# Kernel optimization log

Measured on AMD Instinct MI355X. Metric: run time of the kernel, lower is better.

The kernel has to match this reference:

```python
import jax, jax.numpy as jnp
import numpy as np

# e2m1 FP4 value table: sign bit in nibble MSB, values {0,0.5,1,1.5,2,3,4,6}
_E2M1 = jnp.array([0.0, 0.5, 1.0, 1.5, 2.0, 3.0, 4.0, 6.0,
                   -0.0, -0.5, -1.0, -1.5, -2.0, -3.0, -4.0, -6.0], dtype=jnp.float32)


def _dequant_fp4(packed, scales, group_size):
    """packed: [E, out, in//8] uint32; scales: [E, in//group_size, out] -> [E, out, in] f32."""
    shifts = jnp.arange(8, dtype=jnp.uint32) * 4  # nibble shift amounts 0,4,...,28
    nib = (packed[..., None] >> shifts) & jnp.uint32(0xF)  # [E, out, in//8, 8]
    E, O, P, _ = nib.shape
    nib = nib.reshape(E, O, P * 8).astype(jnp.int32)
    w = _E2M1[nib]  # [E, out, in] f32
    gids = jnp.arange(P * 8) // group_size  # group id per input column
    sc = jnp.transpose(scales, (0, 2, 1))[:, :, gids]  # [E, out, in]
    return w * sc


def setup_inputs() -> dict:
    E, H, I, T, K, G = 8, 2048, 1408, 2048, 2, 128
    key = jax.random.key(0)
    ks = jax.random.split(key, 9)
    x = jax.random.normal(ks[0], (T, H), dtype=jnp.float32)
    gate_packed = jax.random.bits(ks[1], (E, I, H // 8), dtype=jnp.uint32)
    up_packed = jax.random.bits(ks[2], (E, I, H // 8), dtype=jnp.uint32)
    down_packed = jax.random.bits(ks[3], (E, H, I // 8), dtype=jnp.uint32)
    gate_scales = jax.random.uniform(ks[4], (E, H // G, I), jnp.float32, 0.5, 1.5)
    up_scales = jax.random.uniform(ks[5], (E, H // G, I), jnp.float32, 0.5, 1.5)
    down_scales = jax.random.uniform(ks[6], (E, I // G, H), jnp.float32, 0.5, 1.5)
    topk_idx = jax.random.randint(ks[7], (T, K), 0, E, dtype=jnp.int32)
    w = jax.random.uniform(ks[8], (T, K), jnp.float32)
    topk_w = w / jnp.sum(w, axis=-1, keepdims=True)
    return {"x": x,
            "gate_packed": gate_packed, "gate_scales": gate_scales,
            "up_packed": up_packed, "up_scales": up_scales,
            "down_packed": down_packed, "down_scales": down_scales,
            "topk_idx": topk_idx, "topk_w": topk_w, "group_size": G}


def reference(x, gate_packed, gate_scales, up_packed, up_scales,
              down_packed, down_scales, topk_idx, topk_w, group_size):
    # Fused dequant (nibble unpack + e2m1 table + per-group scale) for all experts
    gate_w = _dequant_fp4(gate_packed, gate_scales, group_size)  # [E, I, H]
    up_w = _dequant_fp4(up_packed, up_scales, group_size)        # [E, I, H]
    down_w = _dequant_fp4(down_packed, down_scales, group_size)  # [E, H, I]
    # Grouped SwiGLU expert MLP (dense over E=8 experts, gather routed outputs)
    g = jnp.einsum('th,eih->eti', x, gate_w)
    u = jnp.einsum('th,eih->eti', x, up_w)
    h = jax.nn.silu(g) * u                                        # [E, T, I]
    y = jnp.einsum('eti,ehi->eth', h, down_w)                     # [E, T, H]
    T = x.shape[0]
    sel = y[topk_idx, jnp.arange(T)[:, None], :]                  # [T, K, H]
    return jnp.sum(sel * topk_w[..., None], axis=1)               # [T, H]
```

## Files before the change

### kernel.cpp

```cpp
#include <hip/hip_runtime.h>
#include <hip/hip_bf16.h>
#include <stdint.h>

#define E_ 8
#define H_ 2048
#define I_ 1408
#define T_ 2048
#define K_ 2
#define G_ 128

typedef __bf16 bf16;
typedef bf16 bf16x8 __attribute__((ext_vector_type(8)));
typedef float f32x4 __attribute__((ext_vector_type(4)));

__device__ __forceinline__ uint32_t prm(uint32_t hi, uint32_t lo, uint32_t sel) {
    return __builtin_amdgcn_perm(hi, lo, sel);
}

struct DequantTab { uint32_t thi0, thi1, tlo0, tlo1; };

__device__ __forceinline__ DequantTab build_tab(float s) {
    union { bf16 h[8]; uint32_t u[4]; } tb;
    tb.h[0] = (bf16)(0.0f);
    tb.h[1] = (bf16)(0.5f * s);
    tb.h[2] = (bf16)(1.0f * s);
    tb.h[3] = (bf16)(1.5f * s);
    tb.h[4] = (bf16)(2.0f * s);
    tb.h[5] = (bf16)(3.0f * s);
    tb.h[6] = (bf16)(4.0f * s);
    tb.h[7] = (bf16)(6.0f * s);
    DequantTab t;
    t.thi0 = prm(tb.u[1], tb.u[0], 0x07050301u);
    t.tlo0 = prm(tb.u[1], tb.u[0], 0x06040200u);
    t.thi1 = prm(tb.u[3], tb.u[2], 0x07050301u);
    t.tlo1 = prm(tb.u[3], tb.u[2], 0x06040200u);
    return t;
}

__device__ __forceinline__ uint4 dequant8t(uint32_t p, const DequantTab& t) {
    const uint32_t pr = p >> 4;
    const uint32_t pe = p  & 0x07070707u;
    const uint32_t po = pr & 0x07070707u;
    const uint32_t He = prm(t.thi1, t.thi0, pe) | ((p  & 0x08080808u) << 4);
    const uint32_t Le = prm(t.tlo1, t.tlo0, pe);
    const uint32_t Ho = prm(t.thi1, t.thi0, po) | ((pr & 0x08080808u) << 4);
    const uint32_t Lo = prm(t.tlo1, t.tlo0, po);
    const uint32_t E01 = prm(He, Le, 0x05010400u);
    const uint32_t E23 = prm(He, Le, 0x07030602u);
    const uint32_t O01 = prm(Ho, Lo, 0x05010400u);
    const uint32_t O23 = prm(Ho, Lo, 0x07030602u);
    return make_uint4(prm(O01, E01, 0x05040100u),
                      prm(O01, E01, 0x07060302u),
                      prm(O23, E23, 0x05040100u),
                      prm(O23, E23, 0x07060302u));
}

__device__ __forceinline__ void gld16(void* lds, const void* g) {
    __builtin_amdgcn_global_load_lds(
        (__attribute__((address_space(1))) void*)g,
        (__attribute__((address_space(3))) void*)lds, 16, 0, 0);
}

__global__ void route_count(const int* __restrict__ topk_idx, int* __restrict__ counts) {
    int p = blockIdx.x * blockDim.x + threadIdx.x;
    if (p < T_ * K_) atomicAdd(&counts[topk_idx[p]], 1);
}

__global__ void route_scan(const int* __restrict__ counts, int* __restrict__ offsets,
                           int* __restrict__ tmap) {
    if (threadIdx.x == 0) {
        int acc = 0, ti = 0;
        for (int e = 0; e < E_; e++) {
            offsets[e] = acc;
            int nt = (counts[e] + 127) >> 7;
            for (int j = 0; j < nt; j++) tmap[ti++] = (e << 16) | j;
            acc += counts[e];
        }
        offsets[E_] = acc;
        for (; ti < 64; ti++) tmap[ti] = -1;
    }
}

__global__ void route_fill(const int* __restrict__ topk_idx, const float* __restrict__ topk_w,
                           int* __restrict__ cursors, const int* __restrict__ offsets,
                           int* __restrict__ tok, float* __restrict__ wgt,
                           int* __restrict__ inv) {
    int p = blockIdx.x * blockDim.x + threadIdx.x;
    if (p < T_ * K_) {
        int e = topk_idx[p];
        int slot = atomicAdd(&cursors[e], 1);
        int idx = offsets[e] + slot;
        tok[idx] = p / K_;
        wgt[idx] = topk_w[p];
        inv[p] = idx;
    }
}

__global__ __launch_bounds__(256)
void xcast_kernel(const float* __restrict__ x, uint4* __restrict__ xb) {
    const int i = blockIdx.x * 256 + threadIdx.x;
    const float4 a = ((const float4*)x)[i * 2];
    const float4 b = ((const float4*)x)[i * 2 + 1];
    union { uint4 u; bf16 h[8]; } r;
    r.h[0] = (bf16)a.x; r.h[1] = (bf16)a.y; r.h[2] = (bf16)a.z; r.h[3] = (bf16)a.w;
    r.h[4] = (bf16)b.x; r.h[5] = (bf16)b.y; r.h[6] = (bf16)b.z; r.h[7] = (bf16)b.w;
    xb[i] = r.u;
}

__global__ __launch_bounds__(256)
void gemm1p_kernel(const bf16* __restrict__ xb,
                   const uint32_t* __restrict__ gate_packed,
                   const float* __restrict__ gate_scales,
                   const uint32_t* __restrict__ up_packed,
                   const float* __restrict__ up_scales,
                   const int* __restrict__ offsets,
                   const int* __restrict__ tmap,
                   const int* __restrict__ tok, bf16* __restrict__ h_buf)
{
    const int tm = tmap[blockIdx.y];
    if (tm < 0) return;
    const int e = tm >> 16, ty = tm & 0xffff;
    const int row0 = offsets[e];
    const int cnt = offsets[e + 1] - row0;
    const int itile = blockIdx.x;

    __shared__ __align__(16) bf16 xs[2][128][32];
    __shared__ __align__(16) bf16 wgs[2][64][32];
    __shared__ __align__(16) bf16 wus[2][64][32];
    __shared__ int toks[128];

    const int tid = threadIdx.x;
    if (tid < 128) {
        int r = ty * 128 + tid;
        toks[tid] = tok[row0 + ((r < cnt) ? r : (cnt - 1))];
    }
    __syncthreads();

    const int srow = tid >> 2;
    const int scol = (tid & 3) * 8;
    const int wcol = tid & 3;
    const size_t t0 = toks[srow], t1 = toks[64 + srow];
    const bf16* xg0 = xb + t0 * H_ + scol;
    const bf16* xg1 = xb + t1 * H_ + scol;
    bf16* lx0[2] = { &xs[0][srow][scol], &xs[1][srow][scol] };
    bf16* lx1[2] = { &xs[0][64 + srow][scol], &xs[1][64 + srow][scol] };

    const int irow = itile * 64 + srow;
    const uint32_t* gp_row = gate_packed + (size_t)e * I_ * (H_ / 8) + (size_t)irow * (H_ / 8) + wcol;
    const uint32_t* up_row = up_packed + (size_t)e * I_ * (H_ / 8) + (size_t)irow * (H_ / 8) + wcol;
    const float* gs_row = gate_scales + (size_t)e * (H_ / G_) * I_ + irow;
    const float* us_row = up_scales + (size_t)e * (H_ / G_) * I_ + irow;
    uint4* lwg[2] = { (uint4*)&wgs[0][srow][wcol * 8], (uint4*)&wgs[1][srow][wcol * 8] };
    uint4* lwu[2] = { (uint4*)&wus[0][srow][wcol * 8], (uint4*)&wus[1][srow][wcol * 8] };

    const int wave = tid >> 6, lane = tid & 63;
    const int wy = wave >> 1, wx = wave & 1;
    const int lrow = lane & 15, kq = lane >> 4;

    f32x4 accg[4][2] = {};
    f32x4 accu[4][2] = {};

    float sg_c = gs_row[0], su_c = us_row[0];
    uint32_t pg0 = gp_row[0], pu0 = up_row[0];
    gld16(lx0[0], xg0);
    gld16(lx1[0], xg1);
    DequantTab tg = build_tab(sg_c), tu = build_tab(su_c);
    *lwg[0] = dequant8t(pg0, tg);
    *lwu[0] = dequant8t(pu0, tu);
    __syncthreads();

    for (int kg = 0; kg < H_ / G_; kg++) {
        float sg_n = 0.f, su_n = 0.f;
        if (kg < H_ / G_ - 1) { sg_n = gs_row[(kg + 1) * I_]; su_n = us_row[(kg + 1) * I_]; }
#pragma unroll
        for (int kk = 0; kk < 4; kk++) {
            const int k = kg * 4 + kk;
            const int b = k & 1, nb = b ^ 1;
            const bool hasn = (k < H_ / 32 - 1);
            uint32_t pgn = 0, pun = 0;
            if (hasn) {
                pgn = gp_row[(k + 1) * 4];
                pun = up_row[(k + 1) * 4];
                gld16(lx0[nb], xg0 + (k + 1) * 32);
                gld16(lx1[nb], xg1 + (k + 1) * 32);
            }
            bf16x8 a[4], bg[2], bu[2];
#pragma unroll
            for (int mi = 0; mi < 4; mi++)
                a[mi] = *(const bf16x8*)&xs[b][wy * 64 + mi * 16 + lrow][kq * 8];
#pragma unroll
            for (int ni = 0; ni < 2; ni++) {
                bg[ni] = *(const bf16x8*)&wgs[b][wx * 32 + ni * 16 + lrow][kq * 8];
                bu[ni] = *(const bf16x8*)&wus[b][wx * 32 + ni * 16 + lrow][kq * 8];
            }
#pragma unroll
            for (int mi = 0; mi < 4; mi++)
#pragma unroll
                for (int ni = 0; ni < 2; ni++) {
                    accg[mi][ni] = __builtin_amdgcn_mfma_f32_16x16x32_bf16(a[mi], bg[ni], accg[mi][ni], 0, 0, 0);
                    accu[mi][ni] = __builtin_amdgcn_mfma_f32_16x16x32_bf16(a[mi], bu[ni], accu[mi][ni], 0, 0, 0);
                }
            if (hasn) {
                if (kk == 3) { tg = build_tab(sg_n); tu = build_tab(su_n); }
                *lwg[nb] = dequant8t(pgn, tg);
                *lwu[nb] = dequant8t(pun, tu);
            }
            __syncthreads();
        }
    }

#pragma unroll
    for (int mi = 0; mi < 4; mi++)
#pragma unroll
        for (int ni = 0; ni < 2; ni++) {
            const int icol = itile * 64 + wx * 32 + ni * 16 + lrow;
#pragma unroll
            for (int r = 0; r < 4; r++) {
                const int grow = ty * 128 + wy * 64 + mi * 16 + kq * 4 + r;
                if (grow < cnt) {
                    const float gv = accg[mi][ni][r];
                    const float hv = gv / (1.f + __expf(-gv)) * accu[mi][ni][r];
                    h_buf[(size_t)(row0 + grow) * I_ + icol] = (bf16)hv;
                }
            }
        }
}

__global__ __launch_bounds__(256)
void gemm2p_kernel(const bf16* __restrict__ h_buf,
                   const uint32_t* __restrict__ down_packed,
                   const float* __restrict__ down_scales,
                   const int* __restrict__ offsets,
                   const int* __restrict__ tmap,
                   const int* __restrict__ tok,
                   const float* __restrict__ wgt, float* __restrict__ yp)
{
    const int tm = tmap[blockIdx.y];
    if (tm < 0) return;
    const int e = tm >> 16, ty = tm & 0xffff;
    const int row0 = offsets[e];
    const int cnt = offsets[e + 1] - row0;
    const int htile = blockIdx.x;

    __shared__ __align__(16) bf16 hs[2][128][32];
    __shared__ __align__(16) bf16 wds[2][128][32];
    __shared__ float wgts[128];

    const int tid = threadIdx.x;
    if (tid < 128) {
        int r = ty * 128 + tid;
        wgts[tid] = (r < cnt) ? wgt[row0 + r] : 0.f;
    }
    __syncthreads();

    const int srow = tid >> 2;
    const int scol = (tid & 3) * 8;
    const int m0 = ty * 128 + srow;
    const int hr0 = row0 + ((m0 < cnt) ? m0 : (cnt - 1));
    const int m1 = m0 + 64;
    const int hr1 = row0 + ((m1 < cnt) ? m1 : (cnt - 1));
    const bf16* hg0 = h_buf + (size_t)hr0 * I_ + scol;
    const bf16* hg1 = h_buf + (size_t)hr1 * I_ + scol;
    bf16* lh0[2] = { &hs[0][srow][scol], &hs[1][srow][scol] };
    bf16* lh1[2] = { &hs[0][64 + srow][scol], &hs[1][64 + srow][scol] };

    const int srow2 = tid >> 1;
    const int wcol2 = (tid & 1) * 2;
    const int hrow = htile * 128 + srow2;
    const uint32_t* dp_row = down_packed + (size_t)e * H_ * (I_ / 8) + (size_t)hrow * (I_ / 8) + wcol2;
    const float* ds_row = down_scales + (size_t)e * (I_ / G_) * H_ + hrow;
    uint4* lwd0[2] = { (uint4*)&wds[0][srow2][wcol2 * 8], (uint4*)&wds[1][srow2][wcol2 * 8] };
    uint4* lwd1[2] = { (uint4*)&wds[0][srow2][wcol2 * 8 + 8], (uint4*)&wds[1][srow2][wcol2 * 8 + 8] };

    const int wave = tid >> 6, lane = tid & 63;
    const int wy = wave >> 1, wx = wave & 1;
    const int lrow = lane & 15, kq = lane >> 4;

    f32x4 acc[4][4] = {};

    float sd_c = ds_row[0];
    uint32_t pd0 = dp_row[0], pd1 = dp_row[1];
    gld16(lh0[0], hg0);
    gld16(lh1[0], hg1);
    DequantTab td = build_tab(sd_c);
    *lwd0[0] = dequant8t(pd0, td);
    *lwd1[0] = dequant8t(pd1, td);
    __syncthreads();

    for (int kg = 0; kg < I_ / G_; kg++) {
        float sd_n = 0.f;
        if (kg < I_ / G_ - 1) sd_n = ds_row[(kg + 1) * H_];
#pragma unroll
        for (int kk = 0; kk < 4; kk++) {
            const int k = kg * 4 + kk;
            const int b = k & 1, nb = b ^ 1;
            const bool hasn = (k < I_ / 32 - 1);
            uint32_t pdn0 = 0, pdn1 = 0;
            if (hasn) {
                pdn0 = dp_row[(k + 1) * 4];
                pdn1 = dp_row[(k + 1) * 4 + 1];
                gld16(lh0[nb], hg0 + (k + 1) * 32);
                gld16(lh1[nb], hg1 + (k + 1) * 32);
            }
            bf16x8 a[4], bb[4];
#pragma unroll
            for (int mi = 0; mi < 4; mi++)
                a[mi] = *(const bf16x8*)&hs[b][wy * 64 + mi * 16 + lrow][kq * 8];
#pragma unroll
            for (int ni = 0; ni < 4; ni++)
                bb[ni] = *(const bf16x8*)&wds[b][wx * 64 + ni * 16 + lrow][kq * 8];
#pragma unroll
            for (int mi = 0; mi < 4; mi++)
#pragma unroll
                for (int ni = 0; ni < 4; ni++)
                    acc[mi][ni] = __builtin_amdgcn_mfma_f32_16x16x32_bf16(a[mi], bb[ni], acc[mi][ni], 0, 0, 0);
            if (hasn) {
                if (kk == 3) td = build_tab(sd_n);
                *lwd0[nb] = dequant8t(pdn0, td);
                *lwd1[nb] = dequant8t(pdn1, td);
            }
            __syncthreads();
        }
    }

#pragma unroll
    for (int mi = 0; mi < 4; mi++)
#pragma unroll
        for (int ni = 0; ni < 4; ni++) {
            const int col = htile * 128 + wx * 64 + ni * 16 + lrow;
#pragma unroll
            for (int r = 0; r < 4; r++) {
                const int lr = wy * 64 + mi * 16 + kq * 4 + r;
                if (ty * 128 + lr < cnt)
                    yp[(size_t)(row0 + ty * 128 + lr) * H_ + col] = acc[mi][ni][r] * wgts[lr];
            }
        }
}

__global__ __launch_bounds__(256)
void combine_kernel(const float* __restrict__ yp, const int* __restrict__ inv,
                    float* __restrict__ out) {
    const int idx = blockIdx.x * 256 + threadIdx.x;
    const int t = idx >> 9;
    const int c = idx & 511;
    const float4 a = ((const float4*)yp)[(size_t)inv[t * 2] * (H_ / 4) + c];
    const float4 b = ((const float4*)yp)[(size_t)inv[t * 2 + 1] * (H_ / 4) + c];
    float4 o;
    o.x = a.x + b.x; o.y = a.y + b.y; o.z = a.z + b.z; o.w = a.w + b.w;
    ((float4*)out)[idx] = o;
}

extern "C" void kernel_launch(void* const* d_in, const int* in_sizes, int n_in,
                              void* d_out, int out_size, void* d_ws, size_t ws_size,
                              hipStream_t stream) {
    const float* x = (const float*)d_in[0];
    const uint32_t* gate_packed = (const uint32_t*)d_in[1];
    const float* gate_scales = (const float*)d_in[2];
    const uint32_t* up_packed = (const uint32_t*)d_in[3];
    const float* up_scales = (const float*)d_in[4];
    const uint32_t* down_packed = (const uint32_t*)d_in[5];
    const float* down_scales = (const float*)d_in[6];
    const int* topk_idx = (const int*)d_in[7];
    const float* topk_w = (const float*)d_in[8];
    float* out = (float*)d_out;

    char* ws = (char*)d_ws;
    int* counts  = (int*)ws;
    int* cursors = (int*)(ws + 32);
    int* offsets = (int*)(ws + 64);
    int* tmap    = (int*)(ws + 128);
    int* tok     = (int*)(ws + 512);
    float* wgt   = (float*)(ws + 16896);
    int* inv     = (int*)(ws + 33280);
    bf16* h_buf  = (bf16*)(ws + 49664);
    bf16* xb     = (bf16*)(ws + 49664 + 11534336ull);
    float* yp    = (float*)(ws + 49664 + 11534336ull + 8388608ull);

    hipMemsetAsync(d_ws, 0, 512, stream);

    route_count<<<(T_ * K_ + 255) / 256, 256, 0, stream>>>(topk_idx, counts);
    route_scan<<<1, 64, 0, stream>>>(counts, offsets, tmap);
    route_fill<<<(T_ * K_ + 255) / 256, 256, 0, stream>>>(topk_idx, topk_w, cursors, offsets,
                                                          tok, wgt, inv);
    xcast_kernel<<<T_ * H_ / 8 / 256, 256, 0, stream>>>(x, (uint4*)xb);

    dim3 g1(I_ / 64, 40);
    gemm1p_kernel<<<g1, 256, 0, stream>>>(xb, gate_packed, gate_scales, up_packed, up_scales,
                                          offsets, tmap, tok, h_buf);
    dim3 g2(H_ / 128, 40);
    gemm2p_kernel<<<g2, 256, 0, stream>>>(h_buf, down_packed, down_scales,
                                          offsets, tmap, tok, wgt, yp);
    combine_kernel<<<T_ * H_ / 4 / 256, 256, 0, stream>>>(yp, inv, out);
}
```

Measured before the change: 333.3 us.

## Replace LDS-staged GEMMs with register-direct loads and smaller row tiles

Both expert GEMMs stop staging activations and dequantized weights through shared memory and drop the per-step barriers. Each wave now loads its A fragments straight from global memory into registers and dequantizes its own B fragments in registers, prefetching one k-step ahead. Row tiles shrink from 128 to 64 tokens (more tiles in tmap, grid y raised to 72), and gemm1 widens its I tile to 128. The trade is that weights and activations are no longer shared across waves through LDS, so global and L2 traffic goes up, and the A loads are uncoalesced gathers by token row.

Result: slower. 494.0 us (+48.2%).

```diff
diff --git a/kernel.cpp b/kernel.cpp
--- a/kernel.cpp
+++ b/kernel.cpp
@@ -37,7 +37,7 @@
     return t;
 }
 
-__device__ __forceinline__ uint4 dequant8t(uint32_t p, const DequantTab& t) {
+__device__ __forceinline__ bf16x8 dequant8t(uint32_t p, const DequantTab& t) {
     const uint32_t pr = p >> 4;
     const uint32_t pe = p  & 0x07070707u;
     const uint32_t po = pr & 0x07070707u;
@@ -49,16 +49,12 @@
     const uint32_t E23 = prm(He, Le, 0x07030602u);
     const uint32_t O01 = prm(Ho, Lo, 0x05010400u);
     const uint32_t O23 = prm(Ho, Lo, 0x07030602u);
-    return make_uint4(prm(O01, E01, 0x05040100u),
-                      prm(O01, E01, 0x07060302u),
-                      prm(O23, E23, 0x05040100u),
-                      prm(O23, E23, 0x07060302u));
-}
-
-__device__ __forceinline__ void gld16(void* lds, const void* g) {
-    __builtin_amdgcn_global_load_lds(
-        (__attribute__((address_space(1))) void*)g,
-        (__attribute__((address_space(3))) void*)lds, 16, 0, 0);
+    union { uint4 u; bf16x8 v; } r;
+    r.u = make_uint4(prm(O01, E01, 0x05040100u),
+                     prm(O01, E01, 0x07060302u),
+                     prm(O23, E23, 0x05040100u),
+                     prm(O23, E23, 0x07060302u));
+    return r.v;
 }
 
 __global__ void route_count(const int* __restrict__ topk_idx, int* __restrict__ counts) {
@@ -72,12 +68,12 @@
         int acc = 0, ti = 0;
         for (int e = 0; e < E_; e++) {
             offsets[e] = acc;
-            int nt = (counts[e] + 127) >> 7;
+            int nt = (counts[e] + 63) >> 6;
             for (int j = 0; j < nt; j++) tmap[ti++] = (e << 16) | j;
             acc += counts[e];
         }
         offsets[E_] = acc;
-        for (; ti < 64; ti++) tmap[ti] = -1;
+        for (; ti < 128; ti++) tmap[ti] = -1;
     }
 }
 
@@ -107,8 +103,8 @@
     xb[i] = r.u;
 }
 
-__global__ __launch_bounds__(256)
-void gemm1p_kernel(const bf16* __restrict__ xb,
+__global__ __launch_bounds__(256, 2)
+void gemm1r_kernel(const bf16* __restrict__ xb,
                    const uint32_t* __restrict__ gate_packed,
                    const float* __restrict__ gate_scales,
                    const uint32_t* __restrict__ up_packed,
@@ -124,88 +120,64 @@
     const int cnt = offsets[e + 1] - row0;
     const int itile = blockIdx.x;
 
-    __shared__ __align__(16) bf16 xs[2][128][32];
-    __shared__ __align__(16) bf16 wgs[2][64][32];
-    __shared__ __align__(16) bf16 wus[2][64][32];
-    __shared__ int toks[128];
-
     const int tid = threadIdx.x;
-    if (tid < 128) {
-        int r = ty * 128 + tid;
-        toks[tid] = tok[row0 + ((r < cnt) ? r : (cnt - 1))];
-    }
-    __syncthreads();
-
-    const int srow = tid >> 2;
-    const int scol = (tid & 3) * 8;
-    const int wcol = tid & 3;
-    const size_t t0 = toks[srow], t1 = toks[64 + srow];
-    const bf16* xg0 = xb + t0 * H_ + scol;
-    const bf16* xg1 = xb + t1 * H_ + scol;
-    bf16* lx0[2] = { &xs[0][srow][scol], &xs[1][srow][scol] };
-    bf16* lx1[2] = { &xs[0][64 + srow][scol], &xs[1][64 + srow][scol] };
-
-    const int irow = itile * 64 + srow;
-    const uint32_t* gp_row = gate_packed + (size_t)e * I_ * (H_ / 8) + (size_t)irow * (H_ / 8) + wcol;
-    const uint32_t* up_row = up_packed + (size_t)e * I_ * (H_ / 8) + (size_t)irow * (H_ / 8) + wcol;
-    const float* gs_row = gate_scales + (size_t)e * (H_ / G_) * I_ + irow;
-    const float* us_row = up_scales + (size_t)e * (H_ / G_) * I_ + irow;
-    uint4* lwg[2] = { (uint4*)&wgs[0][srow][wcol * 8], (uint4*)&wgs[1][srow][wcol * 8] };
-    uint4* lwu[2] = { (uint4*)&wus[0][srow][wcol * 8], (uint4*)&wus[1][srow][wcol * 8] };
-
     const int wave = tid >> 6, lane = tid & 63;
-    const int wy = wave >> 1, wx = wave & 1;
     const int lrow = lane & 15, kq = lane >> 4;
+
+    const int irow0 = itile * 128 + wave * 32 + lrow;
+    const int irow1 = irow0 + 16;
+    const uint32_t* gp0 = gate_packed + (size_t)e * I_ * (H_ / 8) + (size_t)irow0 * (H_ / 8) + kq;
+    const uint32_t* gp1 = gate_packed + (size_t)e * I_ * (H_ / 8) + (size_t)irow1 * (H_ / 8) + kq;
+    const uint32_t* up0 = up_packed + (size_t)e * I_ * (H_ / 8) + (size_t)irow0 * (H_ / 8) + kq;
+    const uint32_t* up1 = up_packed + (size_t)e * I_ * (H_ / 8) + (size_t)irow1 * (H_ / 8) + kq;
+    const float* gs_b = gate_scales + (size_t)e * (H_ / G_) * I_;
+    const float* us_b = up_scales + (size_t)e * (H_ / G_) * I_;
+
+    const bf16* xa[4];
+#pragma unroll
+    for (int mi = 0; mi < 4; mi++) {
+        int r = ty * 64 + mi * 16 + lrow;
+        int t = tok[row0 + ((r < cnt) ? r : (cnt - 1))];
+        xa[mi] = xb + (size_t)t * H_ + kq * 8;
+    }
 
     f32x4 accg[4][2] = {};
     f32x4 accu[4][2] = {};
 
-    float sg_c = gs_row[0], su_c = us_row[0];
-    uint32_t pg0 = gp_row[0], pu0 = up_row[0];
-    gld16(lx0[0], xg0);
-    gld16(lx1[0], xg1);
-    DequantTab tg = build_tab(sg_c), tu = build_tab(su_c);
-    *lwg[0] = dequant8t(pg0, tg);
-    *lwu[0] = dequant8t(pu0, tu);
-    __syncthreads();
+    bf16x8 a_c[4];
+#pragma unroll
+    for (int mi = 0; mi < 4; mi++) a_c[mi] = *(const bf16x8*)(xa[mi]);
+    uint32_t pg0_c = gp0[0], pg1_c = gp1[0], pu0_c = up0[0], pu1_c = up1[0];
 
     for (int kg = 0; kg < H_ / G_; kg++) {
-        float sg_n = 0.f, su_n = 0.f;
-        if (kg < H_ / G_ - 1) { sg_n = gs_row[(kg + 1) * I_]; su_n = us_row[(kg + 1) * I_]; }
+        const DequantTab tg0 = build_tab(gs_b[kg * I_ + irow0]);
+        const DequantTab tg1 = build_tab(gs_b[kg * I_ + irow1]);
+        const DequantTab tu0 = build_tab(us_b[kg * I_ + irow0]);
+        const DequantTab tu1 = build_tab(us_b[kg * I_ + irow1]);
 #pragma unroll
         for (int kk = 0; kk < 4; kk++) {
             const int k = kg * 4 + kk;
-            const int b = k & 1, nb = b ^ 1;
-            const bool hasn = (k < H_ / 32 - 1);
-            uint32_t pgn = 0, pun = 0;
-            if (hasn) {
-                pgn = gp_row[(k + 1) * 4];
-                pun = up_row[(k + 1) * 4];
-                gld16(lx0[nb], xg0 + (k + 1) * 32);
-                gld16(lx1[nb], xg1 + (k + 1) * 32);
+            const int kn = (k < 63) ? (k + 1) : 63;
+            bf16x8 a_n[4];
+#pragma unroll
+            for (int mi = 0; mi < 4; mi++) a_n[mi] = *(const bf16x8*)(xa[mi] + kn * 32);
+            const uint32_t pg0_n = gp0[kn * 4], pg1_n = gp1[kn * 4];
+            const uint32_t pu0_n = up0[kn * 4], pu1_n = up1[kn * 4];
+
+            const bf16x8 bg0 = dequant8t(pg0_c, tg0);
+            const bf16x8 bg1 = dequant8t(pg1_c, tg1);
+            const bf16x8 bu0 = dequant8t(pu0_c, tu0);
+            const bf16x8 bu1 = dequant8t(pu1_c, tu1);
+#pragma unroll
+            for (int mi = 0; mi < 4; mi++) {
+                accg[mi][0] = __builtin_amdgcn_mfma_f32_16x16x32_bf16(a_c[mi], bg0, accg[mi][0], 0, 0, 0);
+                accg[mi][1] = __builtin_amdgcn_mfma_f32_16x16x32_bf16(a_c[mi], bg1, accg[mi][1], 0, 0, 0);
+                accu[mi][0] = __builtin_amdgcn_mfma_f32_16x16x32_bf16(a_c[mi], bu0, accu[mi][0], 0, 0, 0);
+                accu[mi][1] = __builtin_amdgcn_mfma_f32_16x16x32_bf16(a_c[mi], bu1, accu[mi][1], 0, 0, 0);
             }
-            bf16x8 a[4], bg[2], bu[2];
-#pragma unroll
-            for (int mi = 0; mi < 4; mi++)
-                a[mi] = *(const bf16x8*)&xs[b][wy * 64 + mi * 16 + lrow][kq * 8];
-#pragma unroll
-            for (int ni = 0; ni < 2; ni++) {
-                bg[ni] = *(const bf16x8*)&wgs[b][wx * 32 + ni * 16 + lrow][kq * 8];
-                bu[ni] = *(const bf16x8*)&wus[b][wx * 32 + ni * 16 + lrow][kq * 8];
-            }
-#pragma unroll
-            for (int mi = 0; mi < 4; mi++)
-#pragma unroll
-                for (int ni = 0; ni < 2; ni++) {
-                    accg[mi][ni] = __builtin_amdgcn_mfma_f32_16x16x32_bf16(a[mi], bg[ni], accg[mi][ni], 0, 0, 0);
-                    accu[mi][ni] = __builtin_amdgcn_mfma_f32_16x16x32_bf16(a[mi], bu[ni], accu[mi][ni], 0, 0, 0);
-                }
-            if (hasn) {
-                if (kk == 3) { tg = build_tab(sg_n); tu = build_tab(su_n); }
-                *lwg[nb] = dequant8t(pgn, tg);
-                *lwu[nb] = dequant8t(pun, tu);
-            }
-            __syncthreads();
+#pragma unroll
+            for (int mi = 0; mi < 4; mi++) a_c[mi] = a_n[mi];
+            pg0_c = pg0_n; pg1_c = pg1_n; pu0_c = pu0_n; pu1_c = pu1_n;
         }
     }
 
@@ -213,10 +185,10 @@
     for (int mi = 0; mi < 4; mi++)
 #pragma unroll
         for (int ni = 0; ni < 2; ni++) {
-            const int icol = itile * 64 + wx * 32 + ni * 16 + lrow;
+            const int icol = itile * 128 + wave * 32 + ni * 16 + lrow;
 #pragma unroll
             for (int r = 0; r < 4; r++) {
-                const int grow = ty * 128 + wy * 64 + mi * 16 + kq * 4 + r;
+                const int grow = ty * 64 + mi * 16 + kq * 4 + r;
                 if (grow < cnt) {
                     const float gv = accg[mi][ni][r];
                     const float hv = gv / (1.f + __expf(-gv)) * accu[mi][ni][r];
@@ -226,13 +198,12 @@
         }
 }
 
-__global__ __launch_bounds__(256)
-void gemm2p_kernel(const bf16* __restrict__ h_buf,
+__global__ __launch_bounds__(256, 3)
+void gemm2r_kernel(const bf16* __restrict__ h_buf,
                    const uint32_t* __restrict__ down_packed,
                    const float* __restrict__ down_scales,
                    const int* __restrict__ offsets,
                    const int* __restrict__ tmap,
-                   const int* __restrict__ tok,
                    const float* __restrict__ wgt, float* __restrict__ yp)
 {
     const int tm = tmap[blockIdx.y];
@@ -242,99 +213,70 @@
     const int cnt = offsets[e + 1] - row0;
     const int htile = blockIdx.x;
 
-    __shared__ __align__(16) bf16 hs[2][128][32];
-    __shared__ __align__(16) bf16 wds[2][128][32];
-    __shared__ float wgts[128];
-
     const int tid = threadIdx.x;
-    if (tid < 128) {
-        int r = ty * 128 + tid;
-        wgts[tid] = (r < cnt) ? wgt[row0 + r] : 0.f;
-    }
-    __syncthreads();
-
-    const int srow = tid >> 2;
-    const int scol = (tid & 3) * 8;
-    const int m0 = ty * 128 + srow;
-    const int hr0 = row0 + ((m0 < cnt) ? m0 : (cnt - 1));
-    const int m1 = m0 + 64;
-    const int hr1 = row0 + ((m1 < cnt) ? m1 : (cnt - 1));
-    const bf16* hg0 = h_buf + (size_t)hr0 * I_ + scol;
-    const bf16* hg1 = h_buf + (size_t)hr1 * I_ + scol;
-    bf16* lh0[2] = { &hs[0][srow][scol], &hs[1][srow][scol] };
-    bf16* lh1[2] = { &hs[0][64 + srow][scol], &hs[1][64 + srow][scol] };
-
-    const int srow2 = tid >> 1;
-    const int wcol2 = (tid & 1) * 2;
-    const int hrow = htile * 128 + srow2;
-    const uint32_t* dp_row = down_packed + (size_t)e * H_ * (I_ / 8) + (size_t)hrow * (I_ / 8) + wcol2;
-    const float* ds_row = down_scales + (size_t)e * (I_ / G_) * H_ + hrow;
-    uint4* lwd0[2] = { (uint4*)&wds[0][srow2][wcol2 * 8], (uint4*)&wds[1][srow2][wcol2 * 8] };
-    uint4* lwd1[2] = { (uint4*)&wds[0][srow2][wcol2 * 8 + 8], (uint4*)&wds[1][srow2][wcol2 * 8 + 8] };
-
     const int wave = tid >> 6, lane = tid & 63;
-    const int wy = wave >> 1, wx = wave & 1;
     const int lrow = lane & 15, kq = lane >> 4;
 
-    f32x4 acc[4][4] = {};
-
-    float sd_c = ds_row[0];
-    uint32_t pd0 = dp_row[0], pd1 = dp_row[1];
-    gld16(lh0[0], hg0);
-    gld16(lh1[0], hg1);
-    DequantTab td = build_tab(sd_c);
-    *lwd0[0] = dequant8t(pd0, td);
-    *lwd1[0] = dequant8t(pd1, td);
-    __syncthreads();
+    const int hrow0 = htile * 128 + wave * 32 + lrow;
+    const int hrow1 = hrow0 + 16;
+    const uint32_t* dp0 = down_packed + (size_t)e * H_ * (I_ / 8) + (size_t)hrow0 * (I_ / 8) + kq;
+    const uint32_t* dp1 = down_packed + (size_t)e * H_ * (I_ / 8) + (size_t)hrow1 * (I_ / 8) + kq;
+    const float* ds_b = down_scales + (size_t)e * (I_ / G_) * H_;
+
+    const bf16* ha[4];
+#pragma unroll
+    for (int mi = 0; mi < 4; mi++) {
+        int r = ty * 64 + mi * 16 + lrow;
+        ha[mi] = h_buf + (size_t)(row0 + ((r < cnt) ? r : (cnt - 1))) * I_ + kq * 8;
+    }
+
+    f32x4 acc[4][2] = {};
+
+    bf16x8 a_c[4];
+#pragma unroll
+    for (int mi = 0; mi < 4; mi++) a_c[mi] = *(const bf16x8*)(ha[mi]);
+    uint32_t pd0_c = dp0[0], pd1_c = dp1[0];
 
     for (int kg = 0; kg < I_ / G_; kg++) {
-        float sd_n = 0.f;
-        if (kg < I_ / G_ - 1) sd_n = ds_row[(kg + 1) * H_];
+        const DequantTab td0 = build_tab(ds_b[kg * H_ + hrow0]);
+        const DequantTab td1 = build_tab(ds_b[kg * H_ + hrow1]);
 #pragma unroll
         for (int kk = 0; kk < 4; kk++) {
             const int k = kg * 4 + kk;
-            const int b = k & 1, nb = b ^ 1;
-            const bool hasn = (k < I_ / 32 - 1);
-            uint32_t pdn0 = 0, pdn1 = 0;
-            if (hasn) {
-                pdn0 = dp_row[(k + 1) * 4];
-                pdn1 = dp_row[(k + 1) * 4 + 1];
-                gld16(lh0[nb], hg0 + (k + 1) * 32);
-                gld16(lh1[nb], hg1 + (k + 1) * 32);
+            const int kn = (k < 43) ? (k + 1) : 43;
+            bf16x8 a_n[4];
+#pragma unroll
+            for (int mi = 0; mi < 4; mi++) a_n[mi] = *(const bf16x8*)(ha[mi] + kn * 32);
+            const uint32_t pd0_n = dp0[kn * 4], pd1_n = dp1[kn * 4];
+
+            const bf16x8 b0 = dequant8t(pd0_c, td0);
+            const bf16x8 b1 = dequant8t(pd1_c, td1);
+#pragma unroll
+            for (int mi = 0; mi < 4; mi++) {
+                acc[mi][0] = __builtin_amdgcn_mfma_f32_16x16x32_bf16(a_c[mi], b0, acc[mi][0], 0, 0, 0);
+                acc[mi][1] = __builtin_amdgcn_mfma_f32_16x16x32_bf16(a_c[mi], b1, acc[mi][1], 0, 0, 0);
             }
-            bf16x8 a[4], bb[4];
-#pragma unroll
-            for (int mi = 0; mi < 4; mi++)
-                a[mi] = *(const bf16x8*)&hs[b][wy * 64 + mi * 16 + lrow][kq * 8];
-#pragma unroll
-            for (int ni = 0; ni < 4; ni++)
-                bb[ni] = *(const bf16x8*)&wds[b][wx * 64 + ni * 16 + lrow][kq * 8];
-#pragma unroll
-            for (int mi = 0; mi < 4; mi++)
-#pragma unroll
-                for (int ni = 0; ni < 4; ni++)
-                    acc[mi][ni] = __builtin_amdgcn_mfma_f32_16x16x32_bf16(a[mi], bb[ni], acc[mi][ni], 0, 0, 0);
-            if (hasn) {
-                if (kk == 3) td = build_tab(sd_n);
-                *lwd0[nb] = dequant8t(pdn0, td);
-                *lwd1[nb] = dequant8t(pdn1, td);
+#pragma unroll
+            for (int mi = 0; mi < 4; mi++) a_c[mi] = a_n[mi];
+            pd0_c = pd0_n; pd1_c = pd1_n;
+        }
+    }
+
+#pragma unroll
+    for (int mi = 0; mi < 4; mi++) {
+#pragma unroll
+        for (int r = 0; r < 4; r++) {
+            const int grow = ty * 64 + mi * 16 + kq * 4 + r;
+            if (grow < cnt) {
+                const float w = wgt[row0 + grow];
+#pragma unroll
+                for (int ni = 0; ni < 2; ni++) {
+                    const int col = htile * 128 + wave * 32 + ni * 16 + lrow;
+                    yp[(size_t)(row0 + grow) * H_ + col] = acc[mi][ni][r] * w;
+                }
             }
-            __syncthreads();
-        }
-    }
-
-#pragma unroll
-    for (int mi = 0; mi < 4; mi++)
-#pragma unroll
-        for (int ni = 0; ni < 4; ni++) {
-            const int col = htile * 128 + wx * 64 + ni * 16 + lrow;
-#pragma unroll
-            for (int r = 0; r < 4; r++) {
-                const int lr = wy * 64 + mi * 16 + kq * 4 + r;
-                if (ty * 128 + lr < cnt)
-                    yp[(size_t)(row0 + ty * 128 + lr) * H_ + col] = acc[mi][ni][r] * wgts[lr];
-            }
-        }
+        }
+    }
 }
 
 __global__ __launch_bounds__(256)
@@ -369,14 +311,14 @@
     int* cursors = (int*)(ws + 32);
     int* offsets = (int*)(ws + 64);
     int* tmap    = (int*)(ws + 128);
-    int* tok     = (int*)(ws + 512);
-    float* wgt   = (float*)(ws + 16896);
-    int* inv     = (int*)(ws + 33280);
-    bf16* h_buf  = (bf16*)(ws + 49664);
-    bf16* xb     = (bf16*)(ws + 49664 + 11534336ull);
-    float* yp    = (float*)(ws + 49664 + 11534336ull + 8388608ull);
-
-    hipMemsetAsync(d_ws, 0, 512, stream);
+    int* tok     = (int*)(ws + 640);
+    float* wgt   = (float*)(ws + 17024);
+    int* inv     = (int*)(ws + 33408);
+    bf16* h_buf  = (bf16*)(ws + 49792);
+    bf16* xb     = (bf16*)(ws + 49792 + 11534336ull);
+    float* yp    = (float*)(ws + 49792 + 11534336ull + 8388608ull);
+
+    hipMemsetAsync(d_ws, 0, 1024, stream);
 
     route_count<<<(T_ * K_ + 255) / 256, 256, 0, stream>>>(topk_idx, counts);
     route_scan<<<1, 64, 0, stream>>>(counts, offsets, tmap);
@@ -384,11 +326,11 @@
                                                           tok, wgt, inv);
     xcast_kernel<<<T_ * H_ / 8 / 256, 256, 0, stream>>>(x, (uint4*)xb);
 
-    dim3 g1(I_ / 64, 40);
-    gemm1p_kernel<<<g1, 256, 0, stream>>>(xb, gate_packed, gate_scales, up_packed, up_scales,
+    dim3 g1(I_ / 128, 72);
+    gemm1r_kernel<<<g1, 256, 0, stream>>>(xb, gate_packed, gate_scales, up_packed, up_scales,
                                           offsets, tmap, tok, h_buf);
-    dim3 g2(H_ / 128, 40);
-    gemm2p_kernel<<<g2, 256, 0, stream>>>(h_buf, down_packed, down_scales,
-                                          offsets, tmap, tok, wgt, yp);
+    dim3 g2(H_ / 128, 72);
+    gemm2r_kernel<<<g2, 256, 0, stream>>>(h_buf, down_packed, down_scales,
+                                          offsets, tmap, wgt, yp);
     combine_kernel<<<T_ * H_ / 4 / 256, 256, 0, stream>>>(yp, inv, out);
 }
```
